# Performance work log

Measured on AMD Instinct MI355X. Metric: run time of the kernel, lower is better.

## Reference

```python
import jax, jax.numpy as jnp
import numpy as np

N = 50000       # nodes
DEG = 16        # fixed degree -> consistent CSR
E = N * DEG     # 800000 edges
IN_FEATS = 256
HEADS = 4
OUT_FEATS = 64
NEG_SLOPE = 0.2


def setup_inputs() -> dict:
    key = jax.random.key(0)
    kx, kc, kw, ki, kj = jax.random.split(key, 5)
    x = jax.random.normal(kx, (N, IN_FEATS), dtype=jnp.float32)
    # consistent CSR: every row has DEG neighbors
    row_id = jnp.repeat(jnp.arange(N, dtype=jnp.int64), DEG)          # [E] dst per edge
    row_ptr = jnp.arange(N + 1, dtype=jnp.int64) * DEG                # [N+1]
    col_id = jax.random.randint(kc, (E,), 0, N, dtype=jnp.int64)      # [E] src per edge
    # glorot-uniform parameters
    def glorot(k, shape, fan_in, fan_out):
        s = float(np.sqrt(6.0 / (fan_in + fan_out)))
        return jax.random.uniform(k, shape, jnp.float32, -s, s)
    W = glorot(kw, (HEADS * OUT_FEATS, IN_FEATS), IN_FEATS, HEADS * OUT_FEATS)  # nn.Linear weight
    att_i = glorot(ki, (1, HEADS, OUT_FEATS), HEADS, OUT_FEATS)
    att_j = glorot(kj, (1, HEADS, OUT_FEATS), HEADS, OUT_FEATS)
    return {"x": x, "row_id": row_id, "row_ptr": row_ptr, "col_id": col_id,
            "W": W, "att_i": att_i, "att_j": att_j}


def reference(x, row_id, row_ptr, col_id, W, att_i, att_j):
    n = x.shape[0]
    H, F = att_i.shape[1], att_i.shape[2]
    # node projection: [N, H, F]
    h = (x @ W.T).reshape(n, H, F)
    # per-node attention halves: [N, H]
    a_i = jnp.sum(h * att_i, axis=-1)   # destination term
    a_j = jnp.sum(h * att_j, axis=-1)   # source term
    # per-edge logits with leaky relu: [E, H]
    e = jax.nn.leaky_relu(a_i[row_id] + a_j[col_id], NEG_SLOPE)
    # segment-wise (per destination row) stable softmax
    m = jax.ops.segment_max(e, row_id, num_segments=n)
    m = jnp.where(jnp.isfinite(m), m, 0.0)
    p = jnp.exp(e - m[row_id])
    s = jax.ops.segment_sum(p, row_id, num_segments=n)
    alpha = p / (s[row_id] + 1e-16)                       # [E, H]
    # weighted scatter-sum of source features: [N, H, F]
    msg = h[col_id] * alpha[:, :, None]
    out = jax.ops.segment_sum(msg, row_id, num_segments=n)
    # concat heads
    return out.reshape(n, H * F)
```

## Files before the change

### kernel.cpp

```cpp
#include <hip/hip_runtime.h>
#include <hip/hip_bf16.h>
#include <stdint.h>

#define N_NODES 50000
#define DEG 16
#define IN_F 256
#define HEADS 4
#define OUT_F 64
#define HF 256
#define NEG_SLOPE 0.2f

typedef short bf16x8 __attribute__((ext_vector_type(8)));
typedef float f32x4 __attribute__((ext_vector_type(4)));

__device__ __forceinline__ unsigned short f2b(float f) {
    __hip_bfloat16 b = __float2bfloat16(f);
    return *(unsigned short*)&b;
}
__device__ __forceinline__ float b2f(unsigned short u) {
    union { uint32_t i; float f; } v; v.i = ((uint32_t)u) << 16;
    return v.f;
}

__global__ __launch_bounds__(256) void wprep(
    const float* __restrict__ W, unsigned short* __restrict__ Wb)
{
    const int i = (blockIdx.x * 256 + threadIdx.x) * 8;
    float4 f0 = ((const float4*)(W + i))[0];
    float4 f1 = ((const float4*)(W + i))[1];
    bf16x8 v;
    v[0] = (short)f2b(f0.x); v[1] = (short)f2b(f0.y);
    v[2] = (short)f2b(f0.z); v[3] = (short)f2b(f0.w);
    v[4] = (short)f2b(f1.x); v[5] = (short)f2b(f1.y);
    v[6] = (short)f2b(f1.z); v[7] = (short)f2b(f1.w);
    *(bf16x8*)(Wb + i) = v;
}

__global__ __launch_bounds__(256) void proj_fused(
    const float* __restrict__ x, const unsigned short* __restrict__ Wb,
    const float* __restrict__ atti, const float* __restrict__ attj,
    unsigned short* __restrict__ h,
    float* __restrict__ a_i, float* __restrict__ a_j)
{
    __shared__ unsigned short As[64 * 256];

    const int tid  = threadIdx.x;
    const int lane = tid & 63;
    const int wave = tid >> 6;
    const int m0   = blockIdx.x * 64;

    #pragma unroll
    for (int p = 0; p < 8; p++) {
        const int C   = p * 256 + tid;
        const int row = C >> 5;
        const int c   = C & 31;
        int grow = m0 + row;
        if (grow >= N_NODES) grow = N_NODES - 1;
        const float* src = x + (size_t)grow * IN_F + c * 8;
        float4 f0 = ((const float4*)src)[0];
        float4 f1 = ((const float4*)src)[1];
        bf16x8 v;
        v[0] = (short)f2b(f0.x); v[1] = (short)f2b(f0.y);
        v[2] = (short)f2b(f0.z); v[3] = (short)f2b(f0.w);
        v[4] = (short)f2b(f1.x); v[5] = (short)f2b(f1.y);
        v[6] = (short)f2b(f1.z); v[7] = (short)f2b(f1.w);
        const int sc = c ^ (row & 7);
        *(bf16x8*)(As + row * 256 + sc * 8) = v;
    }
    __syncthreads();

    const int ar = lane & 15;
    const int kg = lane >> 4;
    const int ncol0 = wave * 64;

    f32x4 acc[4][4];
    #pragma unroll
    for (int i = 0; i < 4; i++)
        #pragma unroll
        for (int j = 0; j < 4; j++)
            #pragma unroll
            for (int k = 0; k < 4; k++) acc[i][j][k] = 0.0f;

    #pragma unroll
    for (int kc8 = 0; kc8 < 8; kc8++) {
        const int kbase = kc8 * 32 + kg * 8;
        const int cA    = kc8 * 4 + kg;
        bf16x8 afrag[4], bfrag[4];
        #pragma unroll
        for (int mi = 0; mi < 4; mi++) {
            const int row = mi * 16 + ar;
            const int sc  = cA ^ (row & 7);
            afrag[mi] = *(const bf16x8*)(As + row * 256 + sc * 8);
        }
        #pragma unroll
        for (int ni = 0; ni < 4; ni++) {
            const int o = ncol0 + ni * 16 + ar;
            bfrag[ni] = *(const bf16x8*)(Wb + (size_t)o * IN_F + kbase);
        }
        #pragma unroll
        for (int mi = 0; mi < 4; mi++)
            #pragma unroll
            for (int ni = 0; ni < 4; ni++)
                acc[mi][ni] = __builtin_amdgcn_mfma_f32_16x16x32_bf16(
                    afrag[mi], bfrag[ni], acc[mi][ni], 0, 0, 0);
    }

    float ai_l[4], aj_l[4];
    #pragma unroll
    for (int ni = 0; ni < 4; ni++) {
        ai_l[ni] = atti[ncol0 + ni * 16 + ar];
        aj_l[ni] = attj[ncol0 + ni * 16 + ar];
    }
    #pragma unroll
    for (int mi = 0; mi < 4; mi++) {
        #pragma unroll
        for (int reg = 0; reg < 4; reg++) {
            const int row = m0 + mi * 16 + kg * 4 + reg;
            float pi = 0.f, pj = 0.f;
            #pragma unroll
            for (int ni = 0; ni < 4; ni++) {
                const float v = acc[mi][ni][reg];
                pi += v * ai_l[ni];
                pj += v * aj_l[ni];
            }
            #pragma unroll
            for (int off = 1; off < 16; off <<= 1) {
                pi += __shfl_xor(pi, off);
                pj += __shfl_xor(pj, off);
            }
            if (row < N_NODES) {
                #pragma unroll
                for (int ni = 0; ni < 4; ni++)
                    h[(size_t)row * HF + ncol0 + ni * 16 + ar] = f2b(acc[mi][ni][reg]);
                if (ar == 0) {
                    a_i[row * HEADS + wave] = pi;
                    a_j[row * HEADS + wave] = pj;
                }
            }
        }
    }
}

__global__ __launch_bounds__(256) void gat_agg(
    const unsigned short* __restrict__ h,
    const float* __restrict__ a_i, const float* __restrict__ a_j,
    const int* __restrict__ col, float* __restrict__ out)
{
    const int lane = threadIdx.x & 63;
    const int node = blockIdx.x * 4 + (threadIdx.x >> 6);
    if (node >= N_NODES) return;
    const int head = lane >> 4;
    const int j = lane & 15;

    const int src = col[node * DEG + j];
    float e = a_i[node * HEADS + head] + a_j[src * HEADS + head];
    e = (e > 0.0f) ? e : NEG_SLOPE * e;
    float m = e;
    #pragma unroll
    for (int off = 1; off < 16; off <<= 1) m = fmaxf(m, __shfl_xor(m, off));
    float p = __expf(e - m);
    float s = p;
    #pragma unroll
    for (int off = 1; off < 16; off <<= 1) s += __shfl_xor(s, off);
    const float alpha = p / (s + 1e-16f);

    float acc0 = 0.f, acc1 = 0.f, acc2 = 0.f, acc3 = 0.f;
    const int myoff = lane * 4;
    #pragma unroll
    for (int jj = 0; jj < 16; jj++) {
        const int sj = __shfl(src, jj);
        const float al = __shfl(alpha, (lane & 48) + jj);
        ushort4 hv = *(const ushort4*)(h + (size_t)sj * HF + myoff);
        acc0 += al * b2f(hv.x);
        acc1 += al * b2f(hv.y);
        acc2 += al * b2f(hv.z);
        acc3 += al * b2f(hv.w);
    }
    float4 o;
    o.x = acc0; o.y = acc1; o.z = acc2; o.w = acc3;
    *(float4*)(out + (size_t)node * HF + myoff) = o;
}

extern "C" void kernel_launch(void* const* d_in, const int* in_sizes, int n_in,
                              void* d_out, int out_size, void* d_ws, size_t ws_size,
                              hipStream_t stream) {
    const float* x      = (const float*)d_in[0];
    const int*   col_id = (const int*)d_in[3];
    const float* W      = (const float*)d_in[4];
    const float* atti   = (const float*)d_in[5];
    const float* attj   = (const float*)d_in[6];
    float* out = (float*)d_out;

    unsigned short* h = (unsigned short*)d_ws;
    float* a_i = (float*)((char*)d_ws + (size_t)N_NODES * HF * 2);
    float* a_j = a_i + (size_t)N_NODES * HEADS;
    unsigned short* Wb = (unsigned short*)(a_j + (size_t)N_NODES * HEADS);

    wprep<<<32, 256, 0, stream>>>(W, Wb);
    proj_fused<<<(N_NODES + 63) / 64, 256, 0, stream>>>(x, Wb, atti, attj, h, a_i, a_j);
    gat_agg<<<(N_NODES + 3) / 4, 256, 0, stream>>>(h, a_i, a_j, col_id, out);
}
```

Before: 191.3 us.

## Map heads to XCD pairs in aggregation and prepack W into MFMA fragments

The aggregation kernel now gives each block one head of four nodes. It picks the head from the XCD index, so each pair of XCDs gathers only one 64-feature slice of h, which should improve L2 hit rates. Inside a block, gathers are ordered in two passes by which half of the node range the source falls in, and col loads and out stores use nontemporal hints. W is repacked once into MFMA fragment order so B-fragment loads are contiguous, and the projection tile shrinks from 64 to 32 rows to launch more blocks. The cost is narrower 2-byte gathers per lane and four times as many aggregation blocks.

```diff
diff --git a/kernel.cpp b/kernel.cpp
--- a/kernel.cpp
+++ b/kernel.cpp
@@ -3,6 +3,7 @@
 #include <stdint.h>
 
 #define N_NODES 50000
+#define HALF_N  25000
 #define DEG 16
 #define IN_F 256
 #define HEADS 4
@@ -23,34 +24,41 @@
 }
 
 __global__ __launch_bounds__(256) void wprep(
-    const float* __restrict__ W, unsigned short* __restrict__ Wb)
+    const float* __restrict__ W, unsigned short* __restrict__ Wbp)
 {
-    const int i = (blockIdx.x * 256 + threadIdx.x) * 8;
-    float4 f0 = ((const float4*)(W + i))[0];
-    float4 f1 = ((const float4*)(W + i))[1];
+    const int G = blockIdx.x * 256 + threadIdx.x;
+    const int cb   = G >> 9;
+    const int rem  = G & 511;
+    const int kc8  = rem >> 6;
+    const int lane = rem & 63;
+    const int kg   = lane >> 4;
+    const int ar   = lane & 15;
+    const float* src = W + (size_t)(cb * 16 + ar) * IN_F + kc8 * 32 + kg * 8;
+    float4 f0 = ((const float4*)src)[0];
+    float4 f1 = ((const float4*)src)[1];
     bf16x8 v;
     v[0] = (short)f2b(f0.x); v[1] = (short)f2b(f0.y);
     v[2] = (short)f2b(f0.z); v[3] = (short)f2b(f0.w);
     v[4] = (short)f2b(f1.x); v[5] = (short)f2b(f1.y);
     v[6] = (short)f2b(f1.z); v[7] = (short)f2b(f1.w);
-    *(bf16x8*)(Wb + i) = v;
+    *(bf16x8*)(Wbp + (size_t)G * 8) = v;
 }
 
 __global__ __launch_bounds__(256) void proj_fused(
-    const float* __restrict__ x, const unsigned short* __restrict__ Wb,
+    const float* __restrict__ x, const unsigned short* __restrict__ Wbp,
     const float* __restrict__ atti, const float* __restrict__ attj,
     unsigned short* __restrict__ h,
     float* __restrict__ a_i, float* __restrict__ a_j)
 {
-    __shared__ unsigned short As[64 * 256];
+    __shared__ unsigned short As[32 * 256];
 
     const int tid  = threadIdx.x;
     const int lane = tid & 63;
     const int wave = tid >> 6;
-    const int m0   = blockIdx.x * 64;
-
-    #pragma unroll
-    for (int p = 0; p < 8; p++) {
+    const int m0   = blockIdx.x * 32;
+
+    #pragma unroll
+    for (int p = 0; p < 4; p++) {
         const int C   = p * 256 + tid;
         const int row = C >> 5;
         const int c   = C & 31;
@@ -73,9 +81,9 @@
     const int kg = lane >> 4;
     const int ncol0 = wave * 64;
 
-    f32x4 acc[4][4];
-    #pragma unroll
-    for (int i = 0; i < 4; i++)
+    f32x4 acc[2][4];
+    #pragma unroll
+    for (int i = 0; i < 2; i++)
         #pragma unroll
         for (int j = 0; j < 4; j++)
             #pragma unroll
@@ -83,22 +91,20 @@
 
     #pragma unroll
     for (int kc8 = 0; kc8 < 8; kc8++) {
-        const int kbase = kc8 * 32 + kg * 8;
-        const int cA    = kc8 * 4 + kg;
-        bf16x8 afrag[4], bfrag[4];
-        #pragma unroll
-        for (int mi = 0; mi < 4; mi++) {
+        bf16x8 afrag[2], bfrag[4];
+        #pragma unroll
+        for (int mi = 0; mi < 2; mi++) {
             const int row = mi * 16 + ar;
-            const int sc  = cA ^ (row & 7);
+            const int sc  = (kc8 * 4 + kg) ^ (row & 7);
             afrag[mi] = *(const bf16x8*)(As + row * 256 + sc * 8);
         }
         #pragma unroll
         for (int ni = 0; ni < 4; ni++) {
-            const int o = ncol0 + ni * 16 + ar;
-            bfrag[ni] = *(const bf16x8*)(Wb + (size_t)o * IN_F + kbase);
-        }
-        #pragma unroll
-        for (int mi = 0; mi < 4; mi++)
+            const int cb = wave * 4 + ni;
+            bfrag[ni] = *(const bf16x8*)(Wbp + ((size_t)(cb * 8 + kc8) * 64 + lane) * 8);
+        }
+        #pragma unroll
+        for (int mi = 0; mi < 2; mi++)
             #pragma unroll
             for (int ni = 0; ni < 4; ni++)
                 acc[mi][ni] = __builtin_amdgcn_mfma_f32_16x16x32_bf16(
@@ -112,7 +118,7 @@
         aj_l[ni] = attj[ncol0 + ni * 16 + ar];
     }
     #pragma unroll
-    for (int mi = 0; mi < 4; mi++) {
+    for (int mi = 0; mi < 2; mi++) {
         #pragma unroll
         for (int reg = 0; reg < 4; reg++) {
             const int row = m0 + mi * 16 + kg * 4 + reg;
@@ -141,44 +147,44 @@
     }
 }
 
-__global__ __launch_bounds__(256) void gat_agg(
+__global__ __launch_bounds__(256) void gat_agg2(
     const unsigned short* __restrict__ h,
     const float* __restrict__ a_i, const float* __restrict__ a_j,
     const int* __restrict__ col, float* __restrict__ out)
 {
+    const int bid  = blockIdx.x;
+    const int xcd  = bid & 7;
+    const int s    = xcd >> 1;
+    const int nb   = ((bid >> 3) << 1) + (bid & 1);
     const int lane = threadIdx.x & 63;
-    const int node = blockIdx.x * 4 + (threadIdx.x >> 6);
-    if (node >= N_NODES) return;
-    const int head = lane >> 4;
-    const int j = lane & 15;
-
-    const int src = col[node * DEG + j];
-    float e = a_i[node * HEADS + head] + a_j[src * HEADS + head];
+    const int node = (nb << 2) + (threadIdx.x >> 6);
+
+    const int j16 = lane & 15;
+    const int src = __builtin_nontemporal_load(col + node * DEG + j16);
+    float e = a_i[node * HEADS + s] + a_j[src * HEADS + s];
     e = (e > 0.0f) ? e : NEG_SLOPE * e;
     float m = e;
     #pragma unroll
     for (int off = 1; off < 16; off <<= 1) m = fmaxf(m, __shfl_xor(m, off));
     float p = __expf(e - m);
-    float s = p;
-    #pragma unroll
-    for (int off = 1; off < 16; off <<= 1) s += __shfl_xor(s, off);
-    const float alpha = p / (s + 1e-16f);
-
-    float acc0 = 0.f, acc1 = 0.f, acc2 = 0.f, acc3 = 0.f;
-    const int myoff = lane * 4;
-    #pragma unroll
-    for (int jj = 0; jj < 16; jj++) {
-        const int sj = __shfl(src, jj);
-        const float al = __shfl(alpha, (lane & 48) + jj);
-        ushort4 hv = *(const ushort4*)(h + (size_t)sj * HF + myoff);
-        acc0 += al * b2f(hv.x);
-        acc1 += al * b2f(hv.y);
-        acc2 += al * b2f(hv.z);
-        acc3 += al * b2f(hv.w);
-    }
-    float4 o;
-    o.x = acc0; o.y = acc1; o.z = acc2; o.w = acc3;
-    *(float4*)(out + (size_t)node * HF + myoff) = o;
+    float sum = p;
+    #pragma unroll
+    for (int off = 1; off < 16; off <<= 1) sum += __shfl_xor(sum, off);
+    const float alpha = p / (sum + 1e-16f);
+
+    float acc = 0.0f;
+    #pragma unroll
+    for (int phase = 0; phase < 2; phase++) {
+        #pragma unroll
+        for (int j = 0; j < 16; j++) {
+            const int sj = __builtin_amdgcn_readfirstlane(__shfl(src, j));
+            if ((int)(sj < HALF_N) != phase) {
+                const float al = __shfl(alpha, j);
+                acc += al * b2f(h[(size_t)sj * HF + s * OUT_F + lane]);
+            }
+        }
+    }
+    __builtin_nontemporal_store(acc, out + (size_t)node * HF + s * OUT_F + lane);
 }
 
 extern "C" void kernel_launch(void* const* d_in, const int* in_sizes, int n_in,
@@ -194,9 +200,9 @@
     unsigned short* h = (unsigned short*)d_ws;
     float* a_i = (float*)((char*)d_ws + (size_t)N_NODES * HF * 2);
     float* a_j = a_i + (size_t)N_NODES * HEADS;
-    unsigned short* Wb = (unsigned short*)(a_j + (size_t)N_NODES * HEADS);
-
-    wprep<<<32, 256, 0, stream>>>(W, Wb);
-    proj_fused<<<(N_NODES + 63) / 64, 256, 0, stream>>>(x, Wb, atti, attj, h, a_i, a_j);
-    gat_agg<<<(N_NODES + 3) / 4, 256, 0, stream>>>(h, a_i, a_j, col_id, out);
-}
+    unsigned short* Wbp = (unsigned short*)(a_j + (size_t)N_NODES * HEADS);
+
+    wprep<<<32, 256, 0, stream>>>(W, Wbp);
+    proj_fused<<<(N_NODES + 31) / 32, 256, 0, stream>>>(x, Wbp, atti, attj, h, a_i, a_j);
+    gat_agg2<<<N_NODES, 256, 0, stream>>>(h, a_i, a_j, col_id, out);
+}
```

Result: slower. 308.2 us (+61.2%).
